# Performance work log

Hardware: AMD Instinct MI355X
Metric: run time of the kernel (lower is better)

## Reference

```python
import jax, jax.numpy as jnp
import numpy as np

B, C_IN, C_OUT, F, K = 4, 64, 64, 50000, 16
BN_EPS = 1e-5


def setup_inputs() -> dict:
    key = jax.random.key(0)
    k1, k2, k3, k4 = jax.random.split(key, 4)
    fea = jax.random.normal(k1, (B, C_IN, F), dtype=jnp.float32)
    ring_n = jax.random.randint(k2, (B, F, K), 0, F, dtype=jnp.int64)
    # Conv1d(kernel_size=1) weight [out, in] and bias [out]
    W = jax.random.normal(k3, (C_OUT, C_IN), dtype=jnp.float32) / np.sqrt(C_IN)
    b = jax.random.normal(k4, (C_OUT,), dtype=jnp.float32) * 0.01
    gamma = jnp.ones((C_OUT,), dtype=jnp.float32)
    beta = jnp.zeros((C_OUT,), dtype=jnp.float32)
    return {"fea": fea, "ring_n": ring_n, "W": W, "b": b, "gamma": gamma, "beta": beta}


def reference(fea, ring_n, W, b, gamma, beta):
    # Note: original torch code overwrites the cat result, so only the
    # NEIGHBOR features are summed (center face excluded).
    def gather_sum(f, r):  # f: [C, F], r: [F, K]
        return f[:, r].sum(axis=-1)  # [C, F, K] -> [C, F]

    summed = jax.vmap(gather_sum)(fea, ring_n)  # [B, C_in, F]
    # 1x1 conv == channel matmul
    y = jnp.einsum("oc,bcf->bof", W, summed) + b[None, :, None]  # [B, C_out, F]
    # BatchNorm1d (training mode): stats over (batch, faces) per channel
    mean = y.mean(axis=(0, 2), keepdims=True)
    var = y.var(axis=(0, 2), keepdims=True)  # biased, as torch BN uses for normalization
    y = (y - mean) * jax.lax.rsqrt(var + BN_EPS)
    y = y * gamma[None, :, None] + beta[None, :, None]
    return jax.nn.relu(y)
```

## Files before the change

kernel.cpp:

```cpp
#include <hip/hip_runtime.h>
#include <hip/hip_bf16.h>
#include <stdint.h>

#define Bn 4
#define Cn 64
#define Fn 50000
#define Kn 16
#define NTOT (Bn*Fn)
#define EPS 1e-5f

typedef unsigned short u16;
typedef unsigned int u32;
typedef __attribute__((ext_vector_type(8))) short short8;
typedef __attribute__((ext_vector_type(4))) float f32x4;

__device__ __forceinline__ u16 f2bf(float x) {
  __hip_bfloat16 h = __float2bfloat16(x);
  return *reinterpret_cast<u16*>(&h);
}
__device__ __forceinline__ u32 pack2(float a, float b) {
  return (u32)f2bf(a) | ((u32)f2bf(b) << 16);
}

__global__ __launch_bounds__(256) void k1_mfma(
    const float* __restrict__ fea, const float* __restrict__ W,
    u32* __restrict__ Gt) {
  const int b = blockIdx.y;
  const int f0 = blockIdx.x * 128;
  const int t = threadIdx.x;
  const int l = t & 63;
  const int quad = l >> 4;
  const int lane15 = l & 15;
  const int wv = t >> 6;
  __shared__ float a_s[64][129];

  short8 afr[4][2];
  #pragma unroll
  for (int ot = 0; ot < 4; ot++) {
    #pragma unroll
    for (int kk = 0; kk < 2; kk++) {
      const float* wr = W + (ot * 16 + lane15) * 64 + kk * 32 + quad * 8;
      float4 wa = *(const float4*)wr;
      float4 wb = *(const float4*)(wr + 4);
      union { short8 v; u32 u[4]; } fr;
      fr.u[0] = pack2(wa.x, wa.y); fr.u[1] = pack2(wa.z, wa.w);
      fr.u[2] = pack2(wb.x, wb.y); fr.u[3] = pack2(wb.z, wb.w);
      afr[ot][kk] = fr.v;
    }
  }

  {
    const float* fb = fea + (size_t)b * Cn * Fn;
    const int f4 = t & 31;
    const int cbase = t >> 5;
    const bool fvalid = (f0 + f4 * 4) < Fn;
    #pragma unroll
    for (int jj = 0; jj < 8; jj++) {
      int c = cbase + jj * 8;
      float4 v = make_float4(0.f, 0.f, 0.f, 0.f);
      if (fvalid) v = *(const float4*)(fb + (size_t)c * Fn + f0 + f4 * 4);
      *(float4*)&a_s[c][f4 * 4] = v;
    }
  }
  __syncthreads();

  f32x4 acc[4][2];
  #pragma unroll
  for (int ot = 0; ot < 4; ot++)
    #pragma unroll
    for (int ft = 0; ft < 2; ft++) acc[ot][ft] = (f32x4){0.f, 0.f, 0.f, 0.f};

  #pragma unroll
  for (int ft = 0; ft < 2; ft++) {
    const int fl = wv * 32 + ft * 16 + lane15;
    float x[16];
    #pragma unroll
    for (int j = 0; j < 8; j++) x[j] = a_s[quad * 8 + j][fl];
    #pragma unroll
    for (int j = 0; j < 8; j++) x[8 + j] = a_s[32 + quad * 8 + j][fl];
    union { short8 s; u32 u[4]; } b0, b1;
    #pragma unroll
    for (int p = 0; p < 4; p++) {
      b0.u[p] = pack2(x[2 * p], x[2 * p + 1]);
      b1.u[p] = pack2(x[8 + 2 * p], x[8 + 2 * p + 1]);
    }
    #pragma unroll
    for (int ot = 0; ot < 4; ot++) {
      acc[ot][ft] = __builtin_amdgcn_mfma_f32_16x16x32_bf16(afr[ot][0], b0.s, acc[ot][ft], 0, 0, 0);
      acc[ot][ft] = __builtin_amdgcn_mfma_f32_16x16x32_bf16(afr[ot][1], b1.s, acc[ot][ft], 0, 0, 0);
    }
  }

  #pragma unroll
  for (int ot = 0; ot < 4; ot++) {
    #pragma unroll
    for (int ft = 0; ft < 2; ft++) {
      int fg = f0 + wv * 32 + ft * 16 + lane15;
      if (fg < Fn) {
        uint2 pv;
        pv.x = pack2(acc[ot][ft][0], acc[ot][ft][1]);
        pv.y = pack2(acc[ot][ft][2], acc[ot][ft][3]);
        *(uint2*)(Gt + ((size_t)(b * 4 + ot) * Fn + fg) * 8 + quad * 2) = pv;
      }
    }
  }
}

template<int WRITE_BF16>
__global__ __launch_bounds__(256) void k2_gather(
    const u32* __restrict__ Gt, const int* __restrict__ ring,
    const float* __restrict__ bias, u32* __restrict__ Y, float* __restrict__ outF,
    float* __restrict__ gsum, float* __restrict__ gsum2) {
  const int bid = blockIdx.x;
  const int combo = bid & 15;
  const int ft = bid >> 4;
  const int b = combo >> 2;
  const int seg = combo & 3;
  const int t = threadIdx.x;
  const int face_l = t >> 1;
  const int half = t & 1;
  const int fa = ft * 128 + face_l;
  const bool valid = fa < Fn;

  __shared__ float y_s[128][17];
  __shared__ float rs[16][17];
  __shared__ float rs2[16][17];

  float acc[8];
  #pragma unroll
  for (int i = 0; i < 8; i++) acc[i] = 0.f;

  const int c0 = seg * 16 + half * 8;
  float bv[8];
  #pragma unroll
  for (int i = 0; i < 8; i++) bv[i] = bias[c0 + i];

  if (valid) {
    const int4* rp = (const int4*)(ring + ((size_t)b * Fn + fa) * Kn);
    int4 i0 = rp[0], i1 = rp[1], i2 = rp[2], i3 = rp[3];
    int idx[16] = {i0.x,i0.y,i0.z,i0.w, i1.x,i1.y,i1.z,i1.w,
                   i2.x,i2.y,i2.z,i2.w, i3.x,i3.y,i3.z,i3.w};
    const uint4* Gs = (const uint4*)(Gt + (size_t)combo * Fn * 8);
    uint4 v[8], w[8];
    #pragma unroll
    for (int k = 0; k < 8; k++) v[k] = Gs[(size_t)idx[k] * 2 + half];
    #pragma unroll
    for (int k = 0; k < 8; k++) w[k] = Gs[(size_t)idx[8 + k] * 2 + half];
    #pragma unroll
    for (int k = 0; k < 8; k++) {
      u32 uu[4] = {v[k].x, v[k].y, v[k].z, v[k].w};
      #pragma unroll
      for (int p = 0; p < 4; p++) {
        acc[2*p]   += __uint_as_float(uu[p] << 16);
        acc[2*p+1] += __uint_as_float(uu[p] & 0xffff0000u);
      }
    }
    #pragma unroll
    for (int k = 0; k < 8; k++) {
      u32 uu[4] = {w[k].x, w[k].y, w[k].z, w[k].w};
      #pragma unroll
      for (int p = 0; p < 4; p++) {
        acc[2*p]   += __uint_as_float(uu[p] << 16);
        acc[2*p+1] += __uint_as_float(uu[p] & 0xffff0000u);
      }
    }
  }
  #pragma unroll
  for (int i = 0; i < 8; i++) acc[i] = valid ? acc[i] + bv[i] : 0.f;
  #pragma unroll
  for (int i = 0; i < 8; i++) y_s[face_l][half * 8 + i] = acc[i];
  __syncthreads();

  if (WRITE_BF16) {
    const int fp = t & 63, chb = t >> 6;
    const int fa2 = ft * 64 + fp;
    if (fa2 * 2 < Fn) {
      #pragma unroll
      for (int j = 0; j < 4; j++) {
        int ch = chb * 4 + j;
        Y[((size_t)b * 64 + seg * 16 + ch) * (Fn / 2) + fa2] =
            pack2(y_s[fp * 2][ch], y_s[fp * 2 + 1][ch]);
      }
    }
  } else {
    const int fl2 = t & 127, chb = t >> 7;
    if (ft * 128 + fl2 < Fn) {
      float* ob = outF + ((size_t)b * 64 + seg * 16 + chb * 8) * Fn + ft * 128 + fl2;
      #pragma unroll
      for (int j = 0; j < 8; j++) ob[(size_t)j * Fn] = y_s[fl2][chb * 8 + j];
    }
  }

  {
    const int ch = t & 15, part = t >> 4;
    float s = 0.f, s2 = 0.f;
    #pragma unroll
    for (int i = 0; i < 8; i++) {
      float v = y_s[part * 8 + i][ch];
      s += v; s2 += v * v;
    }
    rs[part][ch] = s; rs2[part][ch] = s2;
  }
  __syncthreads();
  if (t < 16) {
    float s = 0.f;
    #pragma unroll
    for (int p = 0; p < 16; p++) s += rs[p][t];
    atomicAdd(&gsum[seg * 16 + t], s);
  } else if (t < 32) {
    const int ch = t - 16;
    float s2 = 0.f;
    #pragma unroll
    for (int p = 0; p < 16; p++) s2 += rs2[p][ch];
    atomicAdd(&gsum2[seg * 16 + ch], s2);
  }
}

__global__ void k3_stats(const float* __restrict__ gsum, const float* __restrict__ gsum2,
                         const float* __restrict__ gamma, const float* __restrict__ beta,
                         float* __restrict__ ab) {
  int o = threadIdx.x;
  if (o < 64) {
    float inv = 1.0f / (float)NTOT;
    float mean = gsum[o] * inv;
    float var = gsum2[o] * inv - mean * mean;
    float r = rsqrtf(var + EPS);
    float a = gamma[o] * r;
    ab[o] = a;
    ab[64 + o] = beta[o] - mean * a;
  }
}

__global__ __launch_bounds__(256) void k4_norm_bf(
    const u32* __restrict__ Y, const float* __restrict__ gsum,
    const float* __restrict__ gsum2, const float* __restrict__ gamma,
    const float* __restrict__ beta, float* __restrict__ out) {
  int i = blockIdx.x * 256 + threadIdx.x;
  int ch = (i / 12500) & 63;
  const float inv = 1.0f / (float)NTOT;
  float mean = gsum[ch] * inv;
  float var = gsum2[ch] * inv - mean * mean;
  float a = gamma[ch] * rsqrtf(var + EPS);
  float cc = beta[ch] - mean * a;
  uint2 u = ((const uint2*)Y)[i];
  float4 v;
  v.x = fmaxf(fmaf(__uint_as_float(u.x << 16), a, cc), 0.f);
  v.y = fmaxf(fmaf(__uint_as_float(u.x & 0xffff0000u), a, cc), 0.f);
  v.z = fmaxf(fmaf(__uint_as_float(u.y << 16), a, cc), 0.f);
  v.w = fmaxf(fmaf(__uint_as_float(u.y & 0xffff0000u), a, cc), 0.f);
  ((float4*)out)[i] = v;
}

__global__ __launch_bounds__(256) void k4_norm_f32(float* __restrict__ out,
                                                   const float* __restrict__ ab) {
  int i = blockIdx.x * 256 + threadIdx.x;
  int o = (i / (Fn / 4)) & 63;
  float a = ab[o], c = ab[64 + o];
  float4 v = ((float4*)out)[i];
  v.x = fmaxf(fmaf(v.x, a, c), 0.f);
  v.y = fmaxf(fmaf(v.y, a, c), 0.f);
  v.z = fmaxf(fmaf(v.z, a, c), 0.f);
  v.w = fmaxf(fmaf(v.w, a, c), 0.f);
  ((float4*)out)[i] = v;
}

extern "C" void kernel_launch(void* const* d_in, const int* in_sizes, int n_in,
                              void* d_out, int out_size, void* d_ws, size_t ws_size,
                              hipStream_t stream) {
  const float* fea   = (const float*)d_in[0];
  const int*   ring  = (const int*)d_in[1];
  const float* W     = (const float*)d_in[2];
  const float* bias  = (const float*)d_in[3];
  const float* gamma = (const float*)d_in[4];
  const float* beta  = (const float*)d_in[5];
  float* out = (float*)d_out;

  u32* Gt = (u32*)d_ws;
  const size_t gtBytes = (size_t)Bn * 4 * Fn * 8 * 4;
  const size_t yBytes  = (size_t)Bn * 64 * (Fn / 2) * 4;
  const bool bf16y = ws_size >= gtBytes + yBytes + 1024;

  u32* Y = (u32*)((char*)d_ws + gtBytes);
  float* gsum  = bf16y ? (float*)((char*)d_ws + gtBytes + yBytes)
                       : (float*)((char*)d_ws + gtBytes);
  float* gsum2 = gsum + 64;
  float* ab    = gsum + 128;

  hipMemsetAsync(gsum, 0, 2 * 64 * sizeof(float), stream);
  k1_mfma<<<dim3((Fn + 127) / 128, Bn), 256, 0, stream>>>(fea, W, Gt);
  const int ftiles = (Fn + 127) / 128;
  if (bf16y) {
    k2_gather<1><<<dim3(ftiles * 16), 256, 0, stream>>>(Gt, ring, bias, Y, out, gsum, gsum2);
    k4_norm_bf<<<dim3(Bn * 64 * 12500 / 256), 256, 0, stream>>>(Y, gsum, gsum2, gamma, beta, out);
  } else {
    k2_gather<0><<<dim3(ftiles * 16), 256, 0, stream>>>(Gt, ring, bias, Y, out, gsum, gsum2);
    k3_stats<<<1, 64, 0, stream>>>(gsum, gsum2, gamma, beta, ab);
    k4_norm_f32<<<dim3((Bn * Cn * Fn / 4) / 256), 256, 0, stream>>>(out, ab);
  }
}
```

Baseline: 196.9 us.

## Use face-major 64-channel layout for gathered features and persistent gather blocks

The projected features Gt are now stored face-major, with all 64 channels of a face contiguous (128 bytes). Each gathered neighbor is therefore one full cache line instead of being split across four channel-segment planes, and the ring indices are read once per face rather than four times. The gather kernel becomes a grid-stride persistent loop over 32-face tiles. It keeps per-thread running stats and issues one atomic per channel per block, which cuts atomic traffic. The intermediate Y also becomes face-major, so the normalize kernel now transposes through LDS. k1 stages its output through LDS to write coalesced rows. These changes add extra syncs and LDS work.

```diff
diff --git a/kernel.cpp b/kernel.cpp
--- a/kernel.cpp
+++ b/kernel.cpp
@@ -13,6 +13,8 @@
 typedef unsigned int u32;
 typedef __attribute__((ext_vector_type(8))) short short8;
 typedef __attribute__((ext_vector_type(4))) float f32x4;
+typedef __attribute__((ext_vector_type(4))) int i32x4;
+typedef __attribute__((ext_vector_type(4))) unsigned int u32x4;
 
 __device__ __forceinline__ u16 f2bf(float x) {
   __hip_bfloat16 h = __float2bfloat16(x);
@@ -91,17 +93,27 @@
     }
   }
 
+  __syncthreads();
+  u32* ts = (u32*)&a_s[0][0];
   #pragma unroll
   for (int ot = 0; ot < 4; ot++) {
     #pragma unroll
     for (int ft = 0; ft < 2; ft++) {
-      int fg = f0 + wv * 32 + ft * 16 + lane15;
-      if (fg < Fn) {
-        uint2 pv;
-        pv.x = pack2(acc[ot][ft][0], acc[ot][ft][1]);
-        pv.y = pack2(acc[ot][ft][2], acc[ot][ft][3]);
-        *(uint2*)(Gt + ((size_t)(b * 4 + ot) * Fn + fg) * 8 + quad * 2) = pv;
-      }
+      int fl = wv * 32 + ft * 16 + lane15;
+      uint2 pv;
+      pv.x = pack2(acc[ot][ft][0], acc[ot][ft][1]);
+      pv.y = pack2(acc[ot][ft][2], acc[ot][ft][3]);
+      *(uint2*)&ts[fl * 36 + ot * 8 + quad * 2] = pv;
+    }
+  }
+  __syncthreads();
+  #pragma unroll
+  for (int j = 0; j < 4; j++) {
+    int o = j * 1024 + t * 4;
+    int fl = o >> 5, sl = o & 31;
+    if (f0 + fl < Fn) {
+      u32x4 vv = *(const u32x4*)&ts[fl * 36 + sl];
+      *(u32x4*)(Gt + ((size_t)b * Fn + f0 + fl) * 32 + sl) = vv;
     }
   }
 }
@@ -112,107 +124,118 @@
     const float* __restrict__ bias, u32* __restrict__ Y, float* __restrict__ outF,
     float* __restrict__ gsum, float* __restrict__ gsum2) {
   const int bid = blockIdx.x;
-  const int combo = bid & 15;
-  const int ft = bid >> 4;
-  const int b = combo >> 2;
-  const int seg = combo & 3;
+  const int b = (bid & 7) >> 1;
+  const int sub = ((bid >> 3) << 1) | (bid & 1);
   const int t = threadIdx.x;
-  const int face_l = t >> 1;
-  const int half = t & 1;
-  const int fa = ft * 128 + face_l;
-  const bool valid = fa < Fn;
-
-  __shared__ float y_s[128][17];
-  __shared__ float rs[16][17];
-  __shared__ float rs2[16][17];
-
-  float acc[8];
-  #pragma unroll
-  for (int i = 0; i < 8; i++) acc[i] = 0.f;
-
-  const int c0 = seg * 16 + half * 8;
+  const int gid = t >> 3;
+  const int cs = t & 7;
+  const int sch = t & 63;
+  const int spart = t >> 6;
+
+  __shared__ float y_s[32][65];
+  __shared__ float rs[4][64];
+  __shared__ float rs2[4][64];
+
   float bv[8];
   #pragma unroll
-  for (int i = 0; i < 8; i++) bv[i] = bias[c0 + i];
-
-  if (valid) {
-    const int4* rp = (const int4*)(ring + ((size_t)b * Fn + fa) * Kn);
-    int4 i0 = rp[0], i1 = rp[1], i2 = rp[2], i3 = rp[3];
-    int idx[16] = {i0.x,i0.y,i0.z,i0.w, i1.x,i1.y,i1.z,i1.w,
-                   i2.x,i2.y,i2.z,i2.w, i3.x,i3.y,i3.z,i3.w};
-    const uint4* Gs = (const uint4*)(Gt + (size_t)combo * Fn * 8);
-    uint4 v[8], w[8];
-    #pragma unroll
-    for (int k = 0; k < 8; k++) v[k] = Gs[(size_t)idx[k] * 2 + half];
-    #pragma unroll
-    for (int k = 0; k < 8; k++) w[k] = Gs[(size_t)idx[8 + k] * 2 + half];
-    #pragma unroll
-    for (int k = 0; k < 8; k++) {
-      u32 uu[4] = {v[k].x, v[k].y, v[k].z, v[k].w};
-      #pragma unroll
-      for (int p = 0; p < 4; p++) {
-        acc[2*p]   += __uint_as_float(uu[p] << 16);
-        acc[2*p+1] += __uint_as_float(uu[p] & 0xffff0000u);
+  for (int i = 0; i < 8; i++) bv[i] = bias[cs * 8 + i];
+
+  const u32* Gb = Gt + (size_t)b * Fn * 32;
+  const int* rb = ring + (size_t)b * Fn * Kn;
+
+  float sacc = 0.f, s2acc = 0.f;
+  const int ntiles = (Fn + 31) / 32;
+
+  for (int tile = sub; tile < ntiles; tile += 512) {
+    const int fa = tile * 32 + gid;
+    const bool valid = fa < Fn;
+    float acc[8];
+    #pragma unroll
+    for (int i = 0; i < 8; i++) acc[i] = 0.f;
+
+    if (valid) {
+      const i32x4* rp = (const i32x4*)(rb + (size_t)fa * Kn);
+      i32x4 i0 = __builtin_nontemporal_load(&rp[0]);
+      i32x4 i1 = __builtin_nontemporal_load(&rp[1]);
+      i32x4 i2 = __builtin_nontemporal_load(&rp[2]);
+      i32x4 i3 = __builtin_nontemporal_load(&rp[3]);
+      int idx[16] = {i0[0],i0[1],i0[2],i0[3], i1[0],i1[1],i1[2],i1[3],
+                     i2[0],i2[1],i2[2],i2[3], i3[0],i3[1],i3[2],i3[3]};
+      u32x4 v[8];
+      #pragma unroll
+      for (int k = 0; k < 8; k++)
+        v[k] = *(const u32x4*)(Gb + (size_t)idx[k] * 32 + cs * 4);
+      #pragma unroll
+      for (int k = 0; k < 8; k++) {
+        #pragma unroll
+        for (int p = 0; p < 4; p++) {
+          u32 uu = v[k][p];
+          acc[2*p]   += __uint_as_float(uu << 16);
+          acc[2*p+1] += __uint_as_float(uu & 0xffff0000u);
+        }
       }
-    }
-    #pragma unroll
-    for (int k = 0; k < 8; k++) {
-      u32 uu[4] = {w[k].x, w[k].y, w[k].z, w[k].w};
-      #pragma unroll
-      for (int p = 0; p < 4; p++) {
-        acc[2*p]   += __uint_as_float(uu[p] << 16);
-        acc[2*p+1] += __uint_as_float(uu[p] & 0xffff0000u);
+      u32x4 w[8];
+      #pragma unroll
+      for (int k = 0; k < 8; k++)
+        w[k] = *(const u32x4*)(Gb + (size_t)idx[8 + k] * 32 + cs * 4);
+      #pragma unroll
+      for (int k = 0; k < 8; k++) {
+        #pragma unroll
+        for (int p = 0; p < 4; p++) {
+          u32 uu = w[k][p];
+          acc[2*p]   += __uint_as_float(uu << 16);
+          acc[2*p+1] += __uint_as_float(uu & 0xffff0000u);
+        }
       }
     }
-  }
-  #pragma unroll
-  for (int i = 0; i < 8; i++) acc[i] = valid ? acc[i] + bv[i] : 0.f;
-  #pragma unroll
-  for (int i = 0; i < 8; i++) y_s[face_l][half * 8 + i] = acc[i];
-  __syncthreads();
-
-  if (WRITE_BF16) {
-    const int fp = t & 63, chb = t >> 6;
-    const int fa2 = ft * 64 + fp;
-    if (fa2 * 2 < Fn) {
-      #pragma unroll
-      for (int j = 0; j < 4; j++) {
-        int ch = chb * 4 + j;
-        Y[((size_t)b * 64 + seg * 16 + ch) * (Fn / 2) + fa2] =
-            pack2(y_s[fp * 2][ch], y_s[fp * 2 + 1][ch]);
+
+    float yv[8];
+    #pragma unroll
+    for (int i = 0; i < 8; i++) yv[i] = valid ? acc[i] + bv[i] : 0.f;
+
+    if (WRITE_BF16 && valid) {
+      u32x4 pv;
+      pv[0] = pack2(yv[0], yv[1]); pv[1] = pack2(yv[2], yv[3]);
+      pv[2] = pack2(yv[4], yv[5]); pv[3] = pack2(yv[6], yv[7]);
+      __builtin_nontemporal_store(pv,
+          (u32x4*)(Y + ((size_t)b * Fn + fa) * 32 + cs * 4));
+    }
+
+    #pragma unroll
+    for (int i = 0; i < 8; i++) y_s[gid][cs * 8 + i] = yv[i];
+    __syncthreads();
+    #pragma unroll
+    for (int i = 0; i < 8; i++) {
+      float v = y_s[spart * 8 + i][sch];
+      sacc += v; s2acc += v * v;
+    }
+    if (!WRITE_BF16) {
+      const int ch = t >> 2, q = t & 3;
+      #pragma unroll
+      for (int jj = 0; jj < 2; jj++) {
+        int f4 = q + jj * 4;
+        int fb = tile * 32 + f4 * 4;
+        if (fb < Fn) {
+          float4 wv4;
+          wv4.x = y_s[f4 * 4 + 0][ch]; wv4.y = y_s[f4 * 4 + 1][ch];
+          wv4.z = y_s[f4 * 4 + 2][ch]; wv4.w = y_s[f4 * 4 + 3][ch];
+          *(float4*)(outF + ((size_t)b * 64 + ch) * Fn + fb) = wv4;
+        }
       }
     }
-  } else {
-    const int fl2 = t & 127, chb = t >> 7;
-    if (ft * 128 + fl2 < Fn) {
-      float* ob = outF + ((size_t)b * 64 + seg * 16 + chb * 8) * Fn + ft * 128 + fl2;
-      #pragma unroll
-      for (int j = 0; j < 8; j++) ob[(size_t)j * Fn] = y_s[fl2][chb * 8 + j];
-    }
-  }
-
-  {
-    const int ch = t & 15, part = t >> 4;
-    float s = 0.f, s2 = 0.f;
-    #pragma unroll
-    for (int i = 0; i < 8; i++) {
-      float v = y_s[part * 8 + i][ch];
-      s += v; s2 += v * v;
-    }
-    rs[part][ch] = s; rs2[part][ch] = s2;
-  }
-  __syncthreads();
-  if (t < 16) {
-    float s = 0.f;
-    #pragma unroll
-    for (int p = 0; p < 16; p++) s += rs[p][t];
-    atomicAdd(&gsum[seg * 16 + t], s);
-  } else if (t < 32) {
-    const int ch = t - 16;
-    float s2 = 0.f;
-    #pragma unroll
-    for (int p = 0; p < 16; p++) s2 += rs2[p][ch];
-    atomicAdd(&gsum2[seg * 16 + ch], s2);
+    __syncthreads();
+  }
+
+  rs[spart][sch] = sacc;
+  rs2[spart][sch] = s2acc;
+  __syncthreads();
+  if (t < 64) {
+    float s = rs[0][t] + rs[1][t] + rs[2][t] + rs[3][t];
+    atomicAdd(&gsum[t], s);
+  } else if (t < 128) {
+    const int ch = t - 64;
+    float s2 = rs2[0][ch] + rs2[1][ch] + rs2[2][ch] + rs2[3][ch];
+    atomicAdd(&gsum2[ch], s2);
   }
 }
 
@@ -235,20 +258,47 @@
     const u32* __restrict__ Y, const float* __restrict__ gsum,
     const float* __restrict__ gsum2, const float* __restrict__ gamma,
     const float* __restrict__ beta, float* __restrict__ out) {
-  int i = blockIdx.x * 256 + threadIdx.x;
-  int ch = (i / 12500) & 63;
+  const int b = blockIdx.y;
+  const int f0 = blockIdx.x * 64;
+  const int t = threadIdx.x;
+  __shared__ u32 ys[32][65];
+
+  #pragma unroll
+  for (int j = 0; j < 2; j++) {
+    int o = j * 1024 + t * 4;
+    int fl = o >> 5, sl = o & 31;
+    u32x4 vv = (u32x4)(0u);
+    if (f0 + fl < Fn)
+      vv = *(const u32x4*)(Y + ((size_t)b * Fn + f0 + fl) * 32 + sl);
+    ys[sl + 0][fl] = vv[0]; ys[sl + 1][fl] = vv[1];
+    ys[sl + 2][fl] = vv[2]; ys[sl + 3][fl] = vv[3];
+  }
+  __syncthreads();
+
   const float inv = 1.0f / (float)NTOT;
-  float mean = gsum[ch] * inv;
-  float var = gsum2[ch] * inv - mean * mean;
-  float a = gamma[ch] * rsqrtf(var + EPS);
-  float cc = beta[ch] - mean * a;
-  uint2 u = ((const uint2*)Y)[i];
-  float4 v;
-  v.x = fmaxf(fmaf(__uint_as_float(u.x << 16), a, cc), 0.f);
-  v.y = fmaxf(fmaf(__uint_as_float(u.x & 0xffff0000u), a, cc), 0.f);
-  v.z = fmaxf(fmaf(__uint_as_float(u.y << 16), a, cc), 0.f);
-  v.w = fmaxf(fmaf(__uint_as_float(u.y & 0xffff0000u), a, cc), 0.f);
-  ((float4*)out)[i] = v;
+  const int fi = t & 15, g = t >> 4;
+  const int fbase = 4 * fi;
+  #pragma unroll
+  for (int j = 0; j < 4; j++) {
+    int ch = g * 4 + j;
+    float mean = gsum[ch] * inv;
+    float var = gsum2[ch] * inv - mean * mean;
+    float a = gamma[ch] * rsqrtf(var + EPS);
+    float cc = beta[ch] - mean * a;
+    if (f0 + fbase < Fn) {
+      const int c2 = ch >> 1;
+      const bool hi = ch & 1;
+      float r[4];
+      #pragma unroll
+      for (int rr = 0; rr < 4; rr++) {
+        u32 u = ys[c2][fbase + rr];
+        float xv = __uint_as_float(hi ? (u & 0xffff0000u) : (u << 16));
+        r[rr] = fmaxf(fmaf(xv, a, cc), 0.f);
+      }
+      float4 res = make_float4(r[0], r[1], r[2], r[3]);
+      *(float4*)(out + ((size_t)b * 64 + ch) * Fn + f0 + fbase) = res;
+    }
+  }
 }
 
 __global__ __launch_bounds__(256) void k4_norm_f32(float* __restrict__ out,
@@ -276,11 +326,11 @@
   float* out = (float*)d_out;
 
   u32* Gt = (u32*)d_ws;
-  const size_t gtBytes = (size_t)Bn * 4 * Fn * 8 * 4;
-  const size_t yBytes  = (size_t)Bn * 64 * (Fn / 2) * 4;
+  const size_t gtBytes = (size_t)Bn * Fn * 32 * 4;
+  const size_t yBytes  = (size_t)Bn * Fn * 32 * 4;
   const bool bf16y = ws_size >= gtBytes + yBytes + 1024;
 
-  u32* Y = (u32*)((char*)d_ws + gtBytes);
+  u32* Y = Gt + (size_t)Bn * Fn * 32;
   float* gsum  = bf16y ? (float*)((char*)d_ws + gtBytes + yBytes)
                        : (float*)((char*)d_ws + gtBytes);
   float* gsum2 = gsum + 64;
@@ -288,12 +338,11 @@
 
   hipMemsetAsync(gsum, 0, 2 * 64 * sizeof(float), stream);
   k1_mfma<<<dim3((Fn + 127) / 128, Bn), 256, 0, stream>>>(fea, W, Gt);
-  const int ftiles = (Fn + 127) / 128;
   if (bf16y) {
-    k2_gather<1><<<dim3(ftiles * 16), 256, 0, stream>>>(Gt, ring, bias, Y, out, gsum, gsum2);
-    k4_norm_bf<<<dim3(Bn * 64 * 12500 / 256), 256, 0, stream>>>(Y, gsum, gsum2, gamma, beta, out);
+    k2_gather<1><<<dim3(2048), 256, 0, stream>>>(Gt, ring, bias, Y, out, gsum, gsum2);
+    k4_norm_bf<<<dim3((Fn + 63) / 64, Bn), 256, 0, stream>>>(Y, gsum, gsum2, gamma, beta, out);
   } else {
-    k2_gather<0><<<dim3(ftiles * 16), 256, 0, stream>>>(Gt, ring, bias, Y, out, gsum, gsum2);
+    k2_gather<0><<<dim3(2048), 256, 0, stream>>>(Gt, ring, bias, Y, out, gsum, gsum2);
     k3_stats<<<1, 64, 0, stream>>>(gsum, gsum2, gamma, beta, ab);
     k4_norm_f32<<<dim3((Bn * Cn * Fn / 4) / 256), 256, 0, stream>>>(out, ab);
   }
```

Result: slower. 204.0 us (+3.6%).

## Load features via direct global-to-LDS with swizzle, nontemporal hints, fold memset

Applied to the files above, without the earlier changes.

The k1 feature tile is now loaded with global_load_lds directly into an unpadded LDS array using an XOR swizzle on the face index, replacing register-staged float4 loads and padding. Reads use the matching swizzle to avoid bank conflicts. Ring indices, the bf16 Y intermediate and the final output use nontemporal loads and stores, and the gsum memset is folded into k1 to drop a launch. Out-of-range tail faces now load duplicate data instead of zeros, which is harmless only if those columns are never written.

```diff
diff --git a/kernel.cpp b/kernel.cpp
--- a/kernel.cpp
+++ b/kernel.cpp
@@ -13,6 +13,9 @@
 typedef unsigned int u32;
 typedef __attribute__((ext_vector_type(8))) short short8;
 typedef __attribute__((ext_vector_type(4))) float f32x4;
+typedef __attribute__((ext_vector_type(2))) unsigned int u32x2;
+typedef __attribute__((ext_vector_type(4))) int i32x4;
+typedef __attribute__((ext_vector_type(4))) unsigned int u32x4;
 
 __device__ __forceinline__ u16 f2bf(float x) {
   __hip_bfloat16 h = __float2bfloat16(x);
@@ -21,10 +24,15 @@
 __device__ __forceinline__ u32 pack2(float a, float b) {
   return (u32)f2bf(a) | ((u32)f2bf(b) << 16);
 }
+__device__ __forceinline__ void gload_lds16(const float* g, float* l) {
+  __builtin_amdgcn_global_load_lds(
+      (const __attribute__((address_space(1))) u32*)(g),
+      (__attribute__((address_space(3))) u32*)(l), 16, 0, 0);
+}
 
 __global__ __launch_bounds__(256) void k1_mfma(
     const float* __restrict__ fea, const float* __restrict__ W,
-    u32* __restrict__ Gt) {
+    u32* __restrict__ Gt, float* __restrict__ gsum) {
   const int b = blockIdx.y;
   const int f0 = blockIdx.x * 128;
   const int t = threadIdx.x;
@@ -32,7 +40,21 @@
   const int quad = l >> 4;
   const int lane15 = l & 15;
   const int wv = t >> 6;
-  __shared__ float a_s[64][129];
+  __shared__ float a_s[64 * 128];
+
+  if (blockIdx.x == 0 && b == 0 && t < 128) gsum[t] = 0.f;
+
+  {
+    const float* fb = fea + (size_t)b * Cn * Fn;
+    #pragma unroll
+    for (int i = 0; i < 8; i++) {
+      const int ch = wv * 16 + 2 * i + (l >> 5);
+      const int fblk = (l & 31) ^ ((((ch >> 3) & 3)) << 1);
+      int fg = f0 + fblk * 4;
+      if (fg >= Fn) fg = f0;
+      gload_lds16(fb + (size_t)ch * Fn + fg, &a_s[(wv * 16 + 2 * i) * 128]);
+    }
+  }
 
   short8 afr[4][2];
   #pragma unroll
@@ -48,20 +70,6 @@
       afr[ot][kk] = fr.v;
     }
   }
-
-  {
-    const float* fb = fea + (size_t)b * Cn * Fn;
-    const int f4 = t & 31;
-    const int cbase = t >> 5;
-    const bool fvalid = (f0 + f4 * 4) < Fn;
-    #pragma unroll
-    for (int jj = 0; jj < 8; jj++) {
-      int c = cbase + jj * 8;
-      float4 v = make_float4(0.f, 0.f, 0.f, 0.f);
-      if (fvalid) v = *(const float4*)(fb + (size_t)c * Fn + f0 + f4 * 4);
-      *(float4*)&a_s[c][f4 * 4] = v;
-    }
-  }
   __syncthreads();
 
   f32x4 acc[4][2];
@@ -73,11 +81,12 @@
   #pragma unroll
   for (int ft = 0; ft < 2; ft++) {
     const int fl = wv * 32 + ft * 16 + lane15;
+    const int fsw = fl ^ (quad << 3);
     float x[16];
     #pragma unroll
-    for (int j = 0; j < 8; j++) x[j] = a_s[quad * 8 + j][fl];
-    #pragma unroll
-    for (int j = 0; j < 8; j++) x[8 + j] = a_s[32 + quad * 8 + j][fl];
+    for (int j = 0; j < 8; j++) x[j] = a_s[(quad * 8 + j) * 128 + fsw];
+    #pragma unroll
+    for (int j = 0; j < 8; j++) x[8 + j] = a_s[(32 + quad * 8 + j) * 128 + fsw];
     union { short8 s; u32 u[4]; } b0, b1;
     #pragma unroll
     for (int p = 0; p < 4; p++) {
@@ -136,10 +145,13 @@
   for (int i = 0; i < 8; i++) bv[i] = bias[c0 + i];
 
   if (valid) {
-    const int4* rp = (const int4*)(ring + ((size_t)b * Fn + fa) * Kn);
-    int4 i0 = rp[0], i1 = rp[1], i2 = rp[2], i3 = rp[3];
-    int idx[16] = {i0.x,i0.y,i0.z,i0.w, i1.x,i1.y,i1.z,i1.w,
-                   i2.x,i2.y,i2.z,i2.w, i3.x,i3.y,i3.z,i3.w};
+    const i32x4* rp = (const i32x4*)(ring + ((size_t)b * Fn + fa) * Kn);
+    i32x4 i0 = __builtin_nontemporal_load(&rp[0]);
+    i32x4 i1 = __builtin_nontemporal_load(&rp[1]);
+    i32x4 i2 = __builtin_nontemporal_load(&rp[2]);
+    i32x4 i3 = __builtin_nontemporal_load(&rp[3]);
+    int idx[16] = {i0[0],i0[1],i0[2],i0[3], i1[0],i1[1],i1[2],i1[3],
+                   i2[0],i2[1],i2[2],i2[3], i3[0],i3[1],i3[2],i3[3]};
     const uint4* Gs = (const uint4*)(Gt + (size_t)combo * Fn * 8);
     uint4 v[8], w[8];
     #pragma unroll
@@ -178,8 +190,9 @@
       #pragma unroll
       for (int j = 0; j < 4; j++) {
         int ch = chb * 4 + j;
-        Y[((size_t)b * 64 + seg * 16 + ch) * (Fn / 2) + fa2] =
-            pack2(y_s[fp * 2][ch], y_s[fp * 2 + 1][ch]);
+        u32 pv = pack2(y_s[fp * 2][ch], y_s[fp * 2 + 1][ch]);
+        __builtin_nontemporal_store(pv,
+            Y + ((size_t)b * 64 + seg * 16 + ch) * (Fn / 2) + fa2);
       }
     }
   } else {
@@ -242,13 +255,13 @@
   float var = gsum2[ch] * inv - mean * mean;
   float a = gamma[ch] * rsqrtf(var + EPS);
   float cc = beta[ch] - mean * a;
-  uint2 u = ((const uint2*)Y)[i];
-  float4 v;
-  v.x = fmaxf(fmaf(__uint_as_float(u.x << 16), a, cc), 0.f);
-  v.y = fmaxf(fmaf(__uint_as_float(u.x & 0xffff0000u), a, cc), 0.f);
-  v.z = fmaxf(fmaf(__uint_as_float(u.y << 16), a, cc), 0.f);
-  v.w = fmaxf(fmaf(__uint_as_float(u.y & 0xffff0000u), a, cc), 0.f);
-  ((float4*)out)[i] = v;
+  u32x2 u = __builtin_nontemporal_load((const u32x2*)Y + i);
+  f32x4 v;
+  v[0] = fmaxf(fmaf(__uint_as_float(u[0] << 16), a, cc), 0.f);
+  v[1] = fmaxf(fmaf(__uint_as_float(u[0] & 0xffff0000u), a, cc), 0.f);
+  v[2] = fmaxf(fmaf(__uint_as_float(u[1] << 16), a, cc), 0.f);
+  v[3] = fmaxf(fmaf(__uint_as_float(u[1] & 0xffff0000u), a, cc), 0.f);
+  __builtin_nontemporal_store(v, (f32x4*)out + i);
 }
 
 __global__ __launch_bounds__(256) void k4_norm_f32(float* __restrict__ out,
@@ -286,8 +299,7 @@
   float* gsum2 = gsum + 64;
   float* ab    = gsum + 128;
 
-  hipMemsetAsync(gsum, 0, 2 * 64 * sizeof(float), stream);
-  k1_mfma<<<dim3((Fn + 127) / 128, Bn), 256, 0, stream>>>(fea, W, Gt);
+  k1_mfma<<<dim3((Fn + 127) / 128, Bn), 256, 0, stream>>>(fea, W, Gt, gsum);
   const int ftiles = (Fn + 127) / 128;
   if (bf16y) {
     k2_gather<1><<<dim3(ftiles * 16), 256, 0, stream>>>(Gt, ring, bias, Y, out, gsum, gsum2);
```

Measured after the change: 204.5 us. 3.9% more time.
